# Kernel tuning notes

Measured on AMD Instinct MI355X. Metric: run time of the kernel, lower is better.

The kernel has to match this reference:

```python
import jax, jax.numpy as jnp
import numpy as np
import math

NUM_HEADS = 16


def _alibi_slopes(n):
    # n is a power of 2 here (16)
    start = 2.0 ** (-2.0 ** (-(math.log2(n) - 3)))
    return jnp.asarray([start * (start ** i) for i in range(n)], dtype=jnp.float32)


def setup_inputs() -> dict:
    key = jax.random.key(0)
    ks = jax.random.split(key, 7)
    B, S, D = 2, 2048, 1024
    s = 0.02
    return {
        "query": jax.random.normal(ks[0], (B, S, D), jnp.float32),
        "key": jax.random.normal(ks[1], (B, S, D), jnp.float32),
        "value": jax.random.normal(ks[2], (B, S, D), jnp.float32),
        "Wq": jax.random.normal(ks[3], (D, D), jnp.float32) * s,
        "Wk": jax.random.normal(ks[4], (D, D), jnp.float32) * s,
        "Wv": jax.random.normal(ks[5], (D, D), jnp.float32) * s,
        "Wo": jax.random.normal(ks[6], (D, D), jnp.float32) * s,
    }


def reference(query, key, value, Wq, Wk, Wv, Wo):
    B, S, D = query.shape
    H = NUM_HEADS
    hd = D // H
    scale = math.sqrt(hd)

    # projections (bias-free linears), split into heads: [B, S, H, hd]
    Q = (query @ Wq).reshape(B, S, H, hd)
    K = (key @ Wk).reshape(B, -1, H, hd)
    V = (value @ Wv).reshape(B, -1, H, hd)

    # attention scores [B, H, S, S]
    scores = jnp.einsum("bqhd,bkhd->bhqk", Q, K) / scale

    # ALiBi bias: -slope_h * |i - j|, broadcast over batch
    pos = jnp.arange(S, dtype=jnp.float32)
    rel = jnp.abs(pos[None, :] - pos[:, None])  # [S, S]
    slopes = _alibi_slopes(H)
    scores = scores - slopes[None, :, None, None] * rel[None, None, :, :]

    attn = jax.nn.softmax(scores, axis=-1)
    out = jnp.einsum("bhqk,bkhd->bqhd", attn, V).reshape(B, S, D)
    return out @ Wo
```

## Files before the change

kernel.cpp:

```cpp
#include <hip/hip_runtime.h>
#include <cstdint>
#include <cstddef>


typedef unsigned short u16;
typedef __attribute__((ext_vector_type(8))) _Float16 half8;
typedef __attribute__((ext_vector_type(4))) float f32x4;

#define DEVI static __device__ __forceinline__
#define MFMA16(a, b, c) __builtin_amdgcn_mfma_f32_16x16x32_f16(a, b, c, 0, 0, 0)

DEVI u16 f2h_bits(float f) {
  _Float16 h = (_Float16)f;
  union { _Float16 h; u16 u; } v; v.h = h;
  return v.u;
}

DEVI void gl_lds16(const u16* g, u16* l) {
  __builtin_amdgcn_global_load_lds(
      (const __attribute__((address_space(1))) void*)g,
      (__attribute__((address_space(3))) void*)l, 16, 0, 0);
}

#define LGKM0() __asm__ volatile("s_waitcnt lgkmcnt(0)" ::: "memory")
#define VM0()   __asm__ volatile("s_waitcnt vmcnt(0)" ::: "memory")
#define BARRIER()                       \
  do {                                  \
    __builtin_amdgcn_s_barrier();       \
    __asm__ volatile("" ::: "memory");  \
  } while (0)

__global__ __launch_bounds__(256) void prep(
    const float* __restrict__ q, const float* __restrict__ k,
    const float* __restrict__ v, u16* __restrict__ qb, u16* __restrict__ kb,
    u16* __restrict__ vb, const float* __restrict__ W0,
    const float* __restrict__ W1, const float* __restrict__ W2,
    const float* __restrict__ W3, u16* __restrict__ T0, u16* __restrict__ T1,
    u16* __restrict__ T2, u16* __restrict__ T3, int n) {
  __shared__ float tile[32][33];
  const int z = blockIdx.z;
  if (z < 3) {
    const float* in = z == 0 ? q : (z == 1 ? k : v);
    u16* out = z == 0 ? qb : (z == 1 ? kb : vb);
    int i = (blockIdx.x * 256 + threadIdx.x) * 4;
    if (i + 3 < n) {
      const float4 vv = *(const float4*)(in + i);
      ushort4 o;
      o.x = f2h_bits(vv.x); o.y = f2h_bits(vv.y);
      o.z = f2h_bits(vv.z); o.w = f2h_bits(vv.w);
      *(ushort4*)(out + i) = o;
    }
    return;
  }
  if (blockIdx.x >= 1024) return;
  const int w = z - 3;
  const float* W = w == 0 ? W0 : (w == 1 ? W1 : (w == 2 ? W2 : W3));
  u16* Wt = w == 0 ? T0 : (w == 1 ? T1 : (w == 2 ? T2 : T3));
  const int bx = (blockIdx.x & 31) * 32;
  const int by = (blockIdx.x >> 5) * 32;
  const int x = threadIdx.x & 31;
  const int y0 = threadIdx.x >> 5;
#pragma unroll
  for (int i = y0; i < 32; i += 8)
    tile[i][x] = W[(size_t)(by + i) * 1024 + bx + x];
  __syncthreads();
#pragma unroll
  for (int i = y0; i < 32; i += 8)
    Wt[(size_t)(bx + i) * 1024 + by + x] = f2h_bits(tile[x][i]);
}

DEVI void gemm_body(const u16* __restrict__ A, const u16* __restrict__ Bt,
                    void* __restrict__ Cout, int mode, u16* As, u16* Bs) {
  constexpr int K = 1024, N = 1024;
  const int t = threadIdx.x;
  const int lane = t & 63;
  const int quad = lane >> 4;
  const int l16 = lane & 15;
  const int wid = t >> 6;
  const int g2 = blockIdx.y * 8 + blockIdx.x;
  const int L = (g2 & 7) * 32 + (g2 >> 3);
  const int mBase = (L >> 3) * 128;
  const int nBase = (L & 7) * 128;
  const int wM = (wid >> 1) * 64;
  const int wN = (wid & 1) * 64;
  const int aswz = (quad ^ ((l16 >> 1) & 3)) << 3;

  f32x4 acc[4][4];
#pragma unroll
  for (int i = 0; i < 4; ++i)
#pragma unroll
    for (int j = 0; j < 4; ++j) acc[i][j] = (f32x4){0.f, 0.f, 0.f, 0.f};

  auto stage = [&](int kt, u16* Ad, u16* Bd) {
#pragma unroll
    for (int i = 0; i < 2; ++i) {
      const int ci = i * 256 + t;
      const int row = ci >> 2;
      const int col = (((ci & 3) ^ ((ci >> 3) & 3)) << 3);
      gl_lds16(A + (size_t)(mBase + row) * K + kt * 32 + col, Ad + ci * 8);
      gl_lds16(Bt + (size_t)(nBase + row) * K + kt * 32 + col, Bd + ci * 8);
    }
  };

  u16 *a0 = As, *a1 = As + 4096, *a2 = As + 8192;
  u16 *b0 = Bs, *b1 = Bs + 4096, *b2 = Bs + 8192;

  stage(0, a0, b0);
  stage(1, a1, b1);
  VM0();
  BARRIER();

  for (int kt = 0; kt < K / 32; ++kt) {
    if (kt + 2 < K / 32) stage(kt + 2, a2, b2);

    half8 a[4], b[4];
#pragma unroll
    for (int mi = 0; mi < 4; ++mi)
      a[mi] = *(const half8*)(a0 + (wM + mi * 16 + l16) * 32 + aswz);
#pragma unroll
    for (int ni = 0; ni < 4; ++ni)
      b[ni] = *(const half8*)(b0 + (wN + ni * 16 + l16) * 32 + aswz);
#pragma unroll
    for (int mi = 0; mi < 4; ++mi)
#pragma unroll
      for (int ni = 0; ni < 4; ++ni)
        acc[mi][ni] = MFMA16(a[mi], b[ni], acc[mi][ni]);

    if (kt + 1 < K / 32) {
      if (kt + 2 < K / 32)
        __asm__ volatile("s_waitcnt vmcnt(4)" ::: "memory");
      else
        VM0();
      __builtin_amdgcn_sched_barrier(0);
      LGKM0();
      BARRIER();
    }
    u16* ta = a0; a0 = a1; a1 = a2; a2 = ta;
    u16* tb = b0; b0 = b1; b1 = b2; b2 = tb;
  }

#pragma unroll
  for (int mi = 0; mi < 4; ++mi) {
#pragma unroll
    for (int ni = 0; ni < 4; ++ni) {
#pragma unroll
      for (int r = 0; r < 4; ++r) {
        const int m = mBase + wM + mi * 16 + quad * 4 + r;
        const int n = nBase + wN + ni * 16 + l16;
        const float v = acc[mi][ni][r];
        if (mode == 0) {
          ((float*)Cout)[(size_t)m * N + n] = v;
        } else if (mode == 1) {
          ((u16*)Cout)[(size_t)m * N + n] = f2h_bits(v);
        } else {
          ((u16*)Cout)[(((size_t)(m >> 11) * 1024 + n) << 11) | (size_t)(m & 2047)] = f2h_bits(v);
        }
      }
    }
  }
}

__global__ __launch_bounds__(256) void proj_qkv(
    const u16* __restrict__ qb, const u16* __restrict__ kb, const u16* __restrict__ vb,
    const u16* __restrict__ Wqt, const u16* __restrict__ Wkt, const u16* __restrict__ Wvt,
    u16* __restrict__ Qp, u16* __restrict__ Kp, u16* __restrict__ Vtp) {
  __shared__ u16 As[3 * 128 * 32];
  __shared__ u16 Bs[3 * 128 * 32];
  const int z = blockIdx.z;
  const u16* A = z == 0 ? qb : (z == 1 ? kb : vb);
  const u16* Bt = z == 0 ? Wqt : (z == 1 ? Wkt : Wvt);
  void* C = z == 0 ? (void*)Qp : (z == 1 ? (void*)Kp : (void*)Vtp);
  gemm_body(A, Bt, C, z == 2 ? 2 : 1, As, Bs);
}

__global__ __launch_bounds__(256) void gemm_out(const u16* __restrict__ Ao,
                                                const u16* __restrict__ Wot,
                                                float* __restrict__ out) {
  __shared__ u16 As[3 * 128 * 32];
  __shared__ u16 Bs[3 * 128 * 32];
  gemm_body(Ao, Wot, out, 0, As, Bs);
}

__global__ __launch_bounds__(256, 4) void flash_alibi(
    const u16* __restrict__ Qg, const u16* __restrict__ Kg,
    const u16* __restrict__ Vtg, u16* __restrict__ Og) {
  constexpr int S = 2048, Dm = 1024, HD = 64;
  __shared__ u16 Ks[2][64 * 64];
  __shared__ u16 Vs[2][64 * 64];
  __shared__ u16 Ps[64 * 64];
  const int t = threadIdx.x, lane = t & 63, wid = t >> 6;
  const int quad = lane >> 4, l16 = lane & 15;
  const int qt = blockIdx.x, b = blockIdx.z;
  const int y = blockIdx.y;
  const int h = (y < 8) ? (15 - y) : (y - 8);
  const int qBase = qt * 64;
  const size_t qRow0 = (size_t)b * S + qBase;
  const float sl2 = __builtin_amdgcn_exp2f(-0.5f * (float)(h + 1)) * 1.44269504f;
  const float sc2 = 0.125f * 1.44269504f;
  const int Di = (int)(30.0f / sl2);
  const int ktLo = max(0, (qBase - Di) >> 6);
  const int ktHi = min(31, (qBase + 63 + Di) >> 6);
  const int cswz = ((l16 & 7) << 3);
  const int pRowBase = wid * 16;

#pragma unroll
  for (int i = 0; i < 2; ++i) {
    const int ci = i * 256 + t;
    const int row = ci >> 3, col = (((ci & 7) ^ (row & 7)) << 3);
    gl_lds16(Qg + (qRow0 + row) * Dm + h * HD + col, Ps + ci * 8);
  }
  {
    const int kB = ktLo * 64;
#pragma unroll
    for (int i = 0; i < 2; ++i) {
      const int ci = i * 256 + t;
      const int row = ci >> 3, col = (((ci & 7) ^ (row & 7)) << 3);
      gl_lds16(Kg + ((size_t)b * S + kB + row) * Dm + h * HD + col, Ks[0] + ci * 8);
      gl_lds16(Vtg + ((size_t)(b * 16 + h) * HD + row) * S + kB + col, Vs[0] + ci * 8);
    }
  }

  float bi[4];
#pragma unroll
  for (int r = 0; r < 4; ++r)
    bi[r] = sl2 * (float)(qBase + wid * 16 + quad * 4 + r);

  f32x4 acc_o[4];
#pragma unroll
  for (int nd = 0; nd < 4; ++nd) acc_o[nd] = (f32x4){0.f, 0.f, 0.f, 0.f};
  float lrow[4] = {0.f, 0.f, 0.f, 0.f};

  __syncthreads();

  half8 aq[2];
#pragma unroll
  for (int ks = 0; ks < 2; ++ks) {
    const int ck = ((ks * 4 + quad) << 3) ^ cswz;
    aq[ks] = *(const half8*)(Ps + (pRowBase + l16) * HD + ck);
  }

  int bb = 0;
  for (int kt = ktLo; kt <= ktHi; ++kt) {
    const int kB = kt * 64;
    if (kt < ktHi) {
      const int kBn = kB + 64;
#pragma unroll
      for (int i = 0; i < 2; ++i) {
        const int ci = i * 256 + t;
        const int row = ci >> 3, col = (((ci & 7) ^ (row & 7)) << 3);
        gl_lds16(Kg + ((size_t)b * S + kBn + row) * Dm + h * HD + col, Ks[bb ^ 1] + ci * 8);
        gl_lds16(Vtg + ((size_t)(b * 16 + h) * HD + row) * S + kBn + col, Vs[bb ^ 1] + ci * 8);
      }
    }

    const u16* Kb = Ks[bb];
    const u16* Vb = Vs[bb];

    f32x4 s4[4];
#pragma unroll
    for (int ni = 0; ni < 4; ++ni) s4[ni] = (f32x4){0.f, 0.f, 0.f, 0.f};
    __builtin_amdgcn_s_setprio(1);
#pragma unroll
    for (int ks = 0; ks < 2; ++ks) {
      const int ck = ((ks * 4 + quad) << 3) ^ cswz;
#pragma unroll
      for (int ni = 0; ni < 4; ++ni) {
        const half8 bk = *(const half8*)(Kb + (ni * 16 + l16) * HD + ck);
        s4[ni] = MFMA16(aq[ks], bk, s4[ni]);
      }
    }
    __builtin_amdgcn_s_setprio(0);

    float bj[4];
#pragma unroll
    for (int ni = 0; ni < 4; ++ni) bj[ni] = sl2 * (float)(kB + ni * 16 + l16);
#pragma unroll
    for (int r = 0; r < 4; ++r) {
      float rs = 0.f;
      const int prow = (pRowBase + quad * 4 + r) * 64;
#pragma unroll
      for (int ni = 0; ni < 4; ++ni) {
        const float d = fabsf(bi[r] - bj[ni]);
        const float p = __builtin_amdgcn_exp2f(s4[ni][r] * sc2 - d);
        rs += p;
        Ps[prow + ((ni * 16 + l16) ^ (quad << 4))] = f2h_bits(p);
      }
      lrow[r] += rs;
    }
    __asm__ volatile("s_waitcnt lgkmcnt(0)" ::: "memory");

    __builtin_amdgcn_s_setprio(1);
#pragma unroll
    for (int ks = 0; ks < 2; ++ks) {
      const int pk = (ks * 32 + quad * 8) ^ ((l16 & 12) << 2);
      const int ck = ((ks * 4 + quad) << 3) ^ cswz;
      const half8 aP = *(const half8*)(Ps + (pRowBase + l16) * 64 + pk);
#pragma unroll
      for (int nd = 0; nd < 4; ++nd) {
        const half8 bv = *(const half8*)(Vb + (nd * 16 + l16) * HD + ck);
        acc_o[nd] = MFMA16(aP, bv, acc_o[nd]);
      }
    }
    __builtin_amdgcn_s_setprio(0);

    __syncthreads();
    bb ^= 1;
  }

#pragma unroll
  for (int r = 0; r < 4; ++r) {
    float l = lrow[r];
    l += __shfl_xor(l, 1);
    l += __shfl_xor(l, 2);
    l += __shfl_xor(l, 4);
    l += __shfl_xor(l, 8);
    const float inv = 1.f / l;
    const int rloc = wid * 16 + quad * 4 + r;
#pragma unroll
    for (int nd = 0; nd < 4; ++nd)
      Og[(qRow0 + rloc) * Dm + h * HD + nd * 16 + l16] = f2h_bits(acc_o[nd][r] * inv);
  }
}

extern "C" void kernel_launch(void* const* d_in, const int* in_sizes, int n_in,
                              void* d_out, int out_size, void* d_ws, size_t ws_size,
                              hipStream_t stream) {
  const float* q  = (const float*)d_in[0];
  const float* k  = (const float*)d_in[1];
  const float* v  = (const float*)d_in[2];
  const float* Wq = (const float*)d_in[3];
  const float* Wk = (const float*)d_in[4];
  const float* Wv = (const float*)d_in[5];
  const float* Wo = (const float*)d_in[6];
  char* ws = (char*)d_ws;
  const size_t MB = 1ull << 20;
  u16* qb  = (u16*)(ws + 0 * MB);
  u16* kb  = (u16*)(ws + 8 * MB);
  u16* vb  = (u16*)(ws + 16 * MB);
  u16* Wqt = (u16*)(ws + 24 * MB);
  u16* Wkt = (u16*)(ws + 26 * MB);
  u16* Wvt = (u16*)(ws + 28 * MB);
  u16* Wot = (u16*)(ws + 30 * MB);
  u16* Qp  = (u16*)(ws + 32 * MB);
  u16* Kp  = (u16*)(ws + 40 * MB);
  u16* Vtp = (u16*)(ws + 48 * MB);
  u16* Ao  = (u16*)(ws + 56 * MB);

  const int n = 2 * 2048 * 1024;
  prep<<<dim3(4096, 1, 7), 256, 0, stream>>>(q, k, v, qb, kb, vb,
                                             Wq, Wk, Wv, Wo, Wqt, Wkt, Wvt, Wot, n);
  proj_qkv<<<dim3(8, 32, 3), 256, 0, stream>>>(qb, kb, vb, Wqt, Wkt, Wvt, Qp, Kp, Vtp);
  flash_alibi<<<dim3(32, 16, 2), 256, 0, stream>>>(Qp, Kp, Vtp, Ao);
  gemm_out<<<dim3(8, 32), 256, 0, stream>>>(Ao, Wot, (float*)d_out);
}
```

Baseline: 219.5 us.

## Double flash-attention query tile to 128 rows and compact prep weight-transpose grid

The attention kernel now handles 128 query rows per block, with each wave computing two 16-row MFMA tiles. Each K/V tile loaded into LDS is reused for twice as many query rows, cutting K/V traffic and the number of loop iterations per row. The cost is more registers and LDS (launch bounds lowered to 2 waves per EU), half as many blocks, and wider ALiBi key windows per block. The prep kernel also packs the four weight transposes into one z-slice instead of launching mostly idle z-slices.

```diff
diff --git a/kernel.cpp b/kernel.cpp
--- a/kernel.cpp
+++ b/kernel.cpp
@@ -52,12 +52,12 @@
     }
     return;
   }
-  if (blockIdx.x >= 1024) return;
-  const int w = z - 3;
+  const int w = blockIdx.x >> 10;
+  const int idx = blockIdx.x & 1023;
   const float* W = w == 0 ? W0 : (w == 1 ? W1 : (w == 2 ? W2 : W3));
   u16* Wt = w == 0 ? T0 : (w == 1 ? T1 : (w == 2 ? T2 : T3));
-  const int bx = (blockIdx.x & 31) * 32;
-  const int by = (blockIdx.x >> 5) * 32;
+  const int bx = (idx & 31) * 32;
+  const int by = (idx >> 5) * 32;
   const int x = threadIdx.x & 31;
   const int y0 = threadIdx.x >> 5;
 #pragma unroll
@@ -181,30 +181,31 @@
   gemm_body(Ao, Wot, out, 0, As, Bs);
 }
 
-__global__ __launch_bounds__(256, 4) void flash_alibi(
+__global__ __launch_bounds__(256, 2) void flash_alibi(
     const u16* __restrict__ Qg, const u16* __restrict__ Kg,
     const u16* __restrict__ Vtg, u16* __restrict__ Og) {
   constexpr int S = 2048, Dm = 1024, HD = 64;
   __shared__ u16 Ks[2][64 * 64];
   __shared__ u16 Vs[2][64 * 64];
-  __shared__ u16 Ps[64 * 64];
+  __shared__ u16 Ps[128 * 64];
   const int t = threadIdx.x, lane = t & 63, wid = t >> 6;
   const int quad = lane >> 4, l16 = lane & 15;
-  const int qt = blockIdx.x, b = blockIdx.z;
+  const int qt = blockIdx.x;
   const int y = blockIdx.y;
-  const int h = (y < 8) ? (15 - y) : (y - 8);
-  const int qBase = qt * 64;
+  const int h = (y < 16) ? (15 - (y >> 1)) : ((y - 16) >> 1);
+  const int b = y & 1;
+  const int qBase = qt * 128;
   const size_t qRow0 = (size_t)b * S + qBase;
   const float sl2 = __builtin_amdgcn_exp2f(-0.5f * (float)(h + 1)) * 1.44269504f;
   const float sc2 = 0.125f * 1.44269504f;
   const int Di = (int)(30.0f / sl2);
   const int ktLo = max(0, (qBase - Di) >> 6);
-  const int ktHi = min(31, (qBase + 63 + Di) >> 6);
+  const int ktHi = min(31, (qBase + 127 + Di) >> 6);
   const int cswz = ((l16 & 7) << 3);
-  const int pRowBase = wid * 16;
-
-#pragma unroll
-  for (int i = 0; i < 2; ++i) {
+  const int pRowBase = wid * 32;
+
+#pragma unroll
+  for (int i = 0; i < 4; ++i) {
     const int ci = i * 256 + t;
     const int row = ci >> 3, col = (((ci & 7) ^ (row & 7)) << 3);
     gl_lds16(Qg + (qRow0 + row) * Dm + h * HD + col, Ps + ci * 8);
@@ -220,24 +221,30 @@
     }
   }
 
-  float bi[4];
-#pragma unroll
-  for (int r = 0; r < 4; ++r)
-    bi[r] = sl2 * (float)(qBase + wid * 16 + quad * 4 + r);
-
-  f32x4 acc_o[4];
-#pragma unroll
-  for (int nd = 0; nd < 4; ++nd) acc_o[nd] = (f32x4){0.f, 0.f, 0.f, 0.f};
-  float lrow[4] = {0.f, 0.f, 0.f, 0.f};
+  float bi[2][4];
+#pragma unroll
+  for (int m = 0; m < 2; ++m)
+#pragma unroll
+    for (int r = 0; r < 4; ++r)
+      bi[m][r] = sl2 * (float)(qBase + wid * 32 + m * 16 + quad * 4 + r);
+
+  f32x4 acc_o[2][4];
+#pragma unroll
+  for (int m = 0; m < 2; ++m)
+#pragma unroll
+    for (int nd = 0; nd < 4; ++nd) acc_o[m][nd] = (f32x4){0.f, 0.f, 0.f, 0.f};
+  float lrow[2][4] = {{0.f, 0.f, 0.f, 0.f}, {0.f, 0.f, 0.f, 0.f}};
 
   __syncthreads();
 
-  half8 aq[2];
-#pragma unroll
-  for (int ks = 0; ks < 2; ++ks) {
-    const int ck = ((ks * 4 + quad) << 3) ^ cswz;
-    aq[ks] = *(const half8*)(Ps + (pRowBase + l16) * HD + ck);
-  }
+  half8 aq[2][2];
+#pragma unroll
+  for (int m = 0; m < 2; ++m)
+#pragma unroll
+    for (int ks = 0; ks < 2; ++ks) {
+      const int ck = ((ks * 4 + quad) << 3) ^ cswz;
+      aq[m][ks] = *(const half8*)(Ps + (pRowBase + m * 16 + l16) * HD + ck);
+    }
 
   int bb = 0;
   for (int kt = ktLo; kt <= ktHi; ++kt) {
@@ -256,9 +263,11 @@
     const u16* Kb = Ks[bb];
     const u16* Vb = Vs[bb];
 
-    f32x4 s4[4];
-#pragma unroll
-    for (int ni = 0; ni < 4; ++ni) s4[ni] = (f32x4){0.f, 0.f, 0.f, 0.f};
+    f32x4 s4[2][4];
+#pragma unroll
+    for (int m = 0; m < 2; ++m)
+#pragma unroll
+      for (int ni = 0; ni < 4; ++ni) s4[m][ni] = (f32x4){0.f, 0.f, 0.f, 0.f};
     __builtin_amdgcn_s_setprio(1);
 #pragma unroll
     for (int ks = 0; ks < 2; ++ks) {
@@ -266,7 +275,8 @@
 #pragma unroll
       for (int ni = 0; ni < 4; ++ni) {
         const half8 bk = *(const half8*)(Kb + (ni * 16 + l16) * HD + ck);
-        s4[ni] = MFMA16(aq[ks], bk, s4[ni]);
+        s4[0][ni] = MFMA16(aq[0][ks], bk, s4[0][ni]);
+        s4[1][ni] = MFMA16(aq[1][ks], bk, s4[1][ni]);
       }
     }
     __builtin_amdgcn_s_setprio(0);
@@ -275,17 +285,20 @@
 #pragma unroll
     for (int ni = 0; ni < 4; ++ni) bj[ni] = sl2 * (float)(kB + ni * 16 + l16);
 #pragma unroll
-    for (int r = 0; r < 4; ++r) {
-      float rs = 0.f;
-      const int prow = (pRowBase + quad * 4 + r) * 64;
-#pragma unroll
-      for (int ni = 0; ni < 4; ++ni) {
-        const float d = fabsf(bi[r] - bj[ni]);
-        const float p = __builtin_amdgcn_exp2f(s4[ni][r] * sc2 - d);
-        rs += p;
-        Ps[prow + ((ni * 16 + l16) ^ (quad << 4))] = f2h_bits(p);
-      }
-      lrow[r] += rs;
+    for (int m = 0; m < 2; ++m) {
+#pragma unroll
+      for (int r = 0; r < 4; ++r) {
+        float rs = 0.f;
+        const int prow = (pRowBase + m * 16 + quad * 4 + r) * 64;
+#pragma unroll
+        for (int ni = 0; ni < 4; ++ni) {
+          const float d = fabsf(bi[m][r] - bj[ni]);
+          const float p = __builtin_amdgcn_exp2f(s4[m][ni][r] * sc2 - d);
+          rs += p;
+          Ps[prow + ((ni * 16 + l16) ^ (quad << 4))] = f2h_bits(p);
+        }
+        lrow[m][r] += rs;
+      }
     }
     __asm__ volatile("s_waitcnt lgkmcnt(0)" ::: "memory");
 
@@ -294,11 +307,13 @@
     for (int ks = 0; ks < 2; ++ks) {
       const int pk = (ks * 32 + quad * 8) ^ ((l16 & 12) << 2);
       const int ck = ((ks * 4 + quad) << 3) ^ cswz;
-      const half8 aP = *(const half8*)(Ps + (pRowBase + l16) * 64 + pk);
+      const half8 aP0 = *(const half8*)(Ps + (pRowBase + l16) * 64 + pk);
+      const half8 aP1 = *(const half8*)(Ps + (pRowBase + 16 + l16) * 64 + pk);
 #pragma unroll
       for (int nd = 0; nd < 4; ++nd) {
         const half8 bv = *(const half8*)(Vb + (nd * 16 + l16) * HD + ck);
-        acc_o[nd] = MFMA16(aP, bv, acc_o[nd]);
+        acc_o[0][nd] = MFMA16(aP0, bv, acc_o[0][nd]);
+        acc_o[1][nd] = MFMA16(aP1, bv, acc_o[1][nd]);
       }
     }
     __builtin_amdgcn_s_setprio(0);
@@ -308,17 +323,20 @@
   }
 
 #pragma unroll
-  for (int r = 0; r < 4; ++r) {
-    float l = lrow[r];
-    l += __shfl_xor(l, 1);
-    l += __shfl_xor(l, 2);
-    l += __shfl_xor(l, 4);
-    l += __shfl_xor(l, 8);
-    const float inv = 1.f / l;
-    const int rloc = wid * 16 + quad * 4 + r;
-#pragma unroll
-    for (int nd = 0; nd < 4; ++nd)
-      Og[(qRow0 + rloc) * Dm + h * HD + nd * 16 + l16] = f2h_bits(acc_o[nd][r] * inv);
+  for (int m = 0; m < 2; ++m) {
+#pragma unroll
+    for (int r = 0; r < 4; ++r) {
+      float l = lrow[m][r];
+      l += __shfl_xor(l, 1);
+      l += __shfl_xor(l, 2);
+      l += __shfl_xor(l, 4);
+      l += __shfl_xor(l, 8);
+      const float inv = 1.f / l;
+      const int rloc = wid * 32 + m * 16 + quad * 4 + r;
+#pragma unroll
+      for (int nd = 0; nd < 4; ++nd)
+        Og[(qRow0 + rloc) * Dm + h * HD + nd * 16 + l16] = f2h_bits(acc_o[m][nd][r] * inv);
+    }
   }
 }
 
@@ -347,9 +365,9 @@
   u16* Ao  = (u16*)(ws + 56 * MB);
 
   const int n = 2 * 2048 * 1024;
-  prep<<<dim3(4096, 1, 7), 256, 0, stream>>>(q, k, v, qb, kb, vb,
+  prep<<<dim3(4096, 1, 4), 256, 0, stream>>>(q, k, v, qb, kb, vb,
                                              Wq, Wk, Wv, Wo, Wqt, Wkt, Wvt, Wot, n);
   proj_qkv<<<dim3(8, 32, 3), 256, 0, stream>>>(qb, kb, vb, Wqt, Wkt, Wvt, Qp, Kp, Vtp);
-  flash_alibi<<<dim3(32, 16, 2), 256, 0, stream>>>(Qp, Kp, Vtp, Ao);
+  flash_alibi<<<dim3(16, 32, 1), 256, 0, stream>>>(Qp, Kp, Vtp, Ao);
   gemm_out<<<dim3(8, 32), 256, 0, stream>>>(Ao, Wot, (float*)d_out);
 }
```

Result: no change. 222.7 us (+1.5%).

## Transpose QK^T MFMA operands to vectorize P stores; trim prep grid

Applied to the files above, without the earlier changes.

The attention kernel swaps the MFMA operands so each lane holds four consecutive key columns of one query row. P can then be written to LDS as a packed 8-byte store instead of sixteen scalar stores, and the ALiBi distance is computed from precomputed per-lane offsets. The row-sum reduction now uses two cross-quad shuffles plus an LDS exchange in the epilogue, with the Ps swizzle changed to match. Separately, the prep kernel packs the four weight transposes into z=3 by block index, which removes the idle blocks of the old 7-slice grid.

```diff
diff --git a/kernel.cpp b/kernel.cpp
--- a/kernel.cpp
+++ b/kernel.cpp
@@ -52,12 +52,12 @@
     }
     return;
   }
-  if (blockIdx.x >= 1024) return;
-  const int w = z - 3;
+  const int w = blockIdx.x >> 10;
+  const int idx = blockIdx.x & 1023;
   const float* W = w == 0 ? W0 : (w == 1 ? W1 : (w == 2 ? W2 : W3));
   u16* Wt = w == 0 ? T0 : (w == 1 ? T1 : (w == 2 ? T2 : T3));
-  const int bx = (blockIdx.x & 31) * 32;
-  const int by = (blockIdx.x >> 5) * 32;
+  const int bx = (idx & 31) * 32;
+  const int by = (idx >> 5) * 32;
   const int x = threadIdx.x & 31;
   const int y0 = threadIdx.x >> 5;
 #pragma unroll
@@ -220,15 +220,18 @@
     }
   }
 
-  float bi[4];
-#pragma unroll
-  for (int r = 0; r < 4; ++r)
-    bi[r] = sl2 * (float)(qBase + wid * 16 + quad * 4 + r);
+  const float bQ = sl2 * (float)(qBase + pRowBase + l16);
+  const float sq4 = sl2 * (float)(quad * 4);
+  float cK[4], slr[4];
+#pragma unroll
+  for (int ni = 0; ni < 4; ++ni) cK[ni] = sl2 * (float)(ni * 16);
+#pragma unroll
+  for (int r = 0; r < 4; ++r) slr[r] = sl2 * (float)r;
 
   f32x4 acc_o[4];
 #pragma unroll
   for (int nd = 0; nd < 4; ++nd) acc_o[nd] = (f32x4){0.f, 0.f, 0.f, 0.f};
-  float lrow[4] = {0.f, 0.f, 0.f, 0.f};
+  float lsum = 0.f;
 
   __syncthreads();
 
@@ -266,33 +269,33 @@
 #pragma unroll
       for (int ni = 0; ni < 4; ++ni) {
         const half8 bk = *(const half8*)(Kb + (ni * 16 + l16) * HD + ck);
-        s4[ni] = MFMA16(aq[ks], bk, s4[ni]);
+        s4[ni] = MFMA16(bk, aq[ks], s4[ni]);
       }
     }
     __builtin_amdgcn_s_setprio(0);
 
-    float bj[4];
-#pragma unroll
-    for (int ni = 0; ni < 4; ++ni) bj[ni] = sl2 * (float)(kB + ni * 16 + l16);
-#pragma unroll
-    for (int r = 0; r < 4; ++r) {
-      float rs = 0.f;
-      const int prow = (pRowBase + quad * 4 + r) * 64;
-#pragma unroll
-      for (int ni = 0; ni < 4; ++ni) {
-        const float d = fabsf(bi[r] - bj[ni]);
-        const float p = __builtin_amdgcn_exp2f(s4[ni][r] * sc2 - d);
-        rs += p;
-        Ps[prow + ((ni * 16 + l16) ^ (quad << 4))] = f2h_bits(p);
-      }
-      lrow[r] += rs;
-    }
-    __asm__ volatile("s_waitcnt lgkmcnt(0)" ::: "memory");
+    const float tb = bQ - sl2 * (float)kB - sq4;
+    float rs = 0.f;
+#pragma unroll
+    for (int ni = 0; ni < 4; ++ni) {
+      const float tni = tb - cK[ni];
+      float pv0 = __builtin_amdgcn_exp2f(s4[ni][0] * sc2 - fabsf(tni));
+      float pv1 = __builtin_amdgcn_exp2f(s4[ni][1] * sc2 - fabsf(tni - slr[1]));
+      float pv2 = __builtin_amdgcn_exp2f(s4[ni][2] * sc2 - fabsf(tni - slr[2]));
+      float pv3 = __builtin_amdgcn_exp2f(s4[ni][3] * sc2 - fabsf(tni - slr[3]));
+      rs += (pv0 + pv1) + (pv2 + pv3);
+      uint2 wv;
+      wv.x = (uint32_t)f2h_bits(pv0) | ((uint32_t)f2h_bits(pv1) << 16);
+      wv.y = (uint32_t)f2h_bits(pv2) | ((uint32_t)f2h_bits(pv3) << 16);
+      *(uint2*)(Ps + (pRowBase + l16) * 64 + ((ni * 16 + quad * 4) ^ cswz)) = wv;
+    }
+    lsum += rs;
+    LGKM0();
 
     __builtin_amdgcn_s_setprio(1);
 #pragma unroll
     for (int ks = 0; ks < 2; ++ks) {
-      const int pk = (ks * 32 + quad * 8) ^ ((l16 & 12) << 2);
+      const int pk = (ks * 32 + quad * 8) ^ cswz;
       const int ck = ((ks * 4 + quad) << 3) ^ cswz;
       const half8 aP = *(const half8*)(Ps + (pRowBase + l16) * 64 + pk);
 #pragma unroll
@@ -307,14 +310,15 @@
     bb ^= 1;
   }
 
+  float l = lsum;
+  l += __shfl_xor(l, 16);
+  l += __shfl_xor(l, 32);
+  float* lsh = (float*)Ps + wid * 512;
+  if (quad == 0) lsh[l16] = l;
+  LGKM0();
 #pragma unroll
   for (int r = 0; r < 4; ++r) {
-    float l = lrow[r];
-    l += __shfl_xor(l, 1);
-    l += __shfl_xor(l, 2);
-    l += __shfl_xor(l, 4);
-    l += __shfl_xor(l, 8);
-    const float inv = 1.f / l;
+    const float inv = 1.f / lsh[quad * 4 + r];
     const int rloc = wid * 16 + quad * 4 + r;
 #pragma unroll
     for (int nd = 0; nd < 4; ++nd)
@@ -347,7 +351,7 @@
   u16* Ao  = (u16*)(ws + 56 * MB);
 
   const int n = 2 * 2048 * 1024;
-  prep<<<dim3(4096, 1, 7), 256, 0, stream>>>(q, k, v, qb, kb, vb,
+  prep<<<dim3(4096, 1, 4), 256, 0, stream>>>(q, k, v, qb, kb, vb,
                                              Wq, Wk, Wv, Wo, Wqt, Wkt, Wvt, Wot, n);
   proj_qkv<<<dim3(8, 32, 3), 256, 0, stream>>>(qb, kb, vb, Wqt, Wkt, Wvt, Qp, Kp, Vtp);
   flash_alibi<<<dim3(32, 16, 2), 256, 0, stream>>>(Qp, Kp, Vtp, Ao);
```

Measured after the change: 212.6 us. -3.1%, faster.
